# Performance work log

Measured on AMD Instinct MI355X. Metric: run time of the kernel, lower is better.

Reference implementation:

```python
import jax, jax.numpy as jnp
import numpy as np

B_, L_, D_, N_ = 4, 4096, 64, 16
DT = 0.1
EPS = 1e-6


def _complex_log(x):
    # log|x| (clamped) + i*pi for negative entries, matching torch impl
    real = jnp.log(jnp.maximum(jnp.abs(x), EPS))
    imag = jnp.where(x < 0, jnp.float32(np.pi), jnp.float32(0.0))
    return jax.lax.complex(real, imag)


def _clogaddexp(a, b):
    # stable complex log(exp(a)+exp(b)) using max of real parts
    m = jnp.maximum(a.real, b.real)
    return jnp.log(jnp.exp(a - m) + jnp.exp(b - m)) + m


def _clogcumsumexp(x, axis):
    return jax.lax.associative_scan(_clogaddexp, x, axis=axis)


def setup_inputs() -> dict:
    key = jax.random.key(0)
    ks = jax.random.split(key, 6)
    x = jax.random.normal(ks[0], (B_, L_, D_), jnp.float32)
    s = 1.0 / np.sqrt(D_)
    Wb = jax.random.uniform(ks[1], (N_, D_), jnp.float32, -s, s)
    bb = jax.random.uniform(ks[2], (N_,), jnp.float32, -s, s)
    Wc = jax.random.uniform(ks[3], (N_, D_), jnp.float32, -s, s)
    bc = jax.random.uniform(ks[4], (N_,), jnp.float32, -s, s)
    Wd = jax.random.uniform(ks[5], (1, D_), jnp.float32, -s, s)
    bd = jnp.zeros((1,), jnp.float32)
    # S4D-Real init: A_n = -(n+1), repeated over input_dim rows -> (D, N)
    A = jnp.tile(-(jnp.arange(N_, dtype=jnp.float32) + 1.0)[None, :], (D_, 1))
    return {"x": x, "A": A, "Wb": Wb, "bb": bb, "Wc": Wc, "bc": bc,
            "Wd": Wd, "bd": bd}


def reference(x, A, Wb, bb, Wc, bc, Wd, bd):
    # projections: (b,l,n)
    Bm = x @ Wb.T + bb
    Cm = x @ Wc.T + bc
    # delta network: softplus(linear(x)) + dt, broadcast to input_dim
    delta = jax.nn.softplus(x @ Wd.T + bd) + DT            # (b,l,1)
    dt = jnp.broadcast_to(delta, x.shape)                  # (b,l,d)
    # discretize
    tmp = A * dt[..., None]                                # (b,l,d,n)
    A_bar = jnp.exp(tmp)
    delta_B = jnp.einsum('bld,bln->bldn', dt, Bm)
    B_bar = (A_bar - 1.0) * delta_B / (tmp + EPS)
    term2 = B_bar * x[..., None]                           # (b,l,d,n)
    # parallel scan via complex log-cumsum-exp trick
    log_a = _complex_log(A_bar)
    log_b = _complex_log(term2)
    a_star = jnp.cumsum(log_a, axis=1)                     # (b,l,d,n) complex
    t = _clogcumsumexp(log_b - a_star, axis=1)
    scan = jnp.exp(a_star + t).real                        # (b,l,d,n)
    return jnp.sum(scan * Cm[:, :, None, :], axis=-1)      # (b,l,d)
```

## Files before the change

### kernel.cpp

```cpp
#include <hip/hip_runtime.h>

#define B_ 4
#define L_ 4096
#define D_ 64
#define N_ 16
#define CHUNK 32
#define NCHUNK (L_ / CHUNK)

constexpr float DT_  = 0.1f;
constexpr float EPS_ = 1e-6f;

__global__ __launch_bounds__(64) void proj_kernel(
    const float* __restrict__ x,  const float* __restrict__ A,
    const float* __restrict__ Wb, const float* __restrict__ bb,
    const float* __restrict__ Wc, const float* __restrict__ bc,
    const float* __restrict__ Wd, const float* __restrict__ bd,
    float* __restrict__ P, float* __restrict__ Cm)
{
    const int bl   = blockIdx.x;
    const int lane = threadIdx.x;

    float xd = x[(size_t)bl * D_ + lane];
    __shared__ float xs[D_];
    xs[lane] = xd;

    float p = xd * Wd[lane];
    #pragma unroll
    for (int m = 32; m >= 1; m >>= 1) p += __shfl_xor(p, m, 64);
    float z = p + bd[0];
    float delta = fmaxf(z, 0.0f) + log1pf(expf(-fabsf(z))) + DT_;

    __syncthreads();

    if (lane < 32) {
        const int n = lane & 15;
        const float* W  = (lane < 16) ? Wb : Wc;
        float acc = (lane < 16) ? bb[n] : bc[n];
        #pragma unroll
        for (int d = 0; d < D_; d++) acc += xs[d] * W[n * D_ + d];

        if (lane < 16) {
            float An  = A[n];
            float tmp = An * delta;
            float a   = expf(tmp);
            float g   = (a - 1.0f) * delta * acc / (tmp + EPS_);
            P[(size_t)bl * 32 + n]      = a;
            P[(size_t)bl * 32 + 16 + n] = g;
        } else {
            Cm[(size_t)bl * 16 + n] = acc;
        }
    }
}

__global__ __launch_bounds__(64) void scan_local(
    const float* __restrict__ x, const float* __restrict__ P,
    float* __restrict__ S, float* __restrict__ Cdec)
{
    const int b = blockIdx.x / NCHUNK;
    const int c = blockIdx.x % NCHUNK;
    const int d = threadIdx.x;

    float h[N_], cum[N_];
    #pragma unroll
    for (int n = 0; n < N_; n++) { h[n] = 0.0f; cum[n] = 1.0f; }

    const int l0 = c * CHUNK;
    for (int l = l0; l < l0 + CHUNK; l++) {
        const int base = b * L_ + l;
        float xd = x[(size_t)base * D_ + d];
        const float* pp = P + (size_t)base * 32;
        #pragma unroll
        for (int n = 0; n < N_; n++) {
            float a = pp[n];
            float g = pp[16 + n];
            h[n]   = a * h[n] + g * xd;
            cum[n] *= a;
        }
    }

    const int sbase = (b * NCHUNK + c) * N_;
    #pragma unroll
    for (int n = 0; n < N_; n++)
        S[(size_t)(sbase + n) * D_ + d] = h[n];
    if (d == 0) {
        #pragma unroll
        for (int n = 0; n < N_; n++) Cdec[sbase + n] = cum[n];
    }
}

__global__ __launch_bounds__(256) void combine(
    float* __restrict__ S, const float* __restrict__ Cdec)
{
    const int g = blockIdx.x * 256 + threadIdx.x;
    const int b = g / (N_ * D_);
    const int r = g % (N_ * D_);
    const int n = r / D_;
    const int d = r % D_;

    float run = 0.0f;
    for (int c = 0; c < NCHUNK; c++) {
        const size_t idx = (size_t)((b * NCHUNK + c) * N_ + n) * D_ + d;
        float s = S[idx];
        S[idx] = run;
        run = Cdec[(b * NCHUNK + c) * N_ + n] * run + s;
    }
}

__global__ __launch_bounds__(64) void scan_out(
    const float* __restrict__ x, const float* __restrict__ P,
    const float* __restrict__ Cmat, const float* __restrict__ S,
    float* __restrict__ out)
{
    const int b = blockIdx.x / NCHUNK;
    const int c = blockIdx.x % NCHUNK;
    const int d = threadIdx.x;

    float h[N_];
    const int sbase = (b * NCHUNK + c) * N_;
    #pragma unroll
    for (int n = 0; n < N_; n++)
        h[n] = S[(size_t)(sbase + n) * D_ + d];

    const int l0 = c * CHUNK;
    for (int l = l0; l < l0 + CHUNK; l++) {
        const int base = b * L_ + l;
        float xd = x[(size_t)base * D_ + d];
        const float* pp = P + (size_t)base * 32;
        const float* cc = Cmat + (size_t)base * 16;
        float acc = 0.0f;
        #pragma unroll
        for (int n = 0; n < N_; n++) {
            float a = pp[n];
            float g = pp[16 + n];
            h[n] = a * h[n] + g * xd;
            acc += cc[n] * h[n];
        }
        out[(size_t)base * D_ + d] = acc;
    }
}

extern "C" void kernel_launch(void* const* d_in, const int* in_sizes, int n_in,
                              void* d_out, int out_size, void* d_ws, size_t ws_size,
                              hipStream_t stream)
{
    const float* x  = (const float*)d_in[0];
    const float* A  = (const float*)d_in[1];
    const float* Wb = (const float*)d_in[2];
    const float* bb = (const float*)d_in[3];
    const float* Wc = (const float*)d_in[4];
    const float* bc = (const float*)d_in[5];
    const float* Wd = (const float*)d_in[6];
    const float* bd = (const float*)d_in[7];
    float* out = (float*)d_out;

    float* P    = (float*)d_ws;
    float* Cm   = P  + (size_t)B_ * L_ * 32;
    float* S    = Cm + (size_t)B_ * L_ * 16;
    float* Cdec = S  + (size_t)B_ * NCHUNK * N_ * D_;

    proj_kernel<<<B_ * L_, 64, 0, stream>>>(x, A, Wb, bb, Wc, bc, Wd, bd, P, Cm);
    scan_local<<<B_ * NCHUNK, 64, 0, stream>>>(x, P, S, Cdec);
    combine<<<(B_ * N_ * D_) / 256, 256, 0, stream>>>(S, Cdec);
    scan_out<<<B_ * NCHUNK, 64, 0, stream>>>(x, P, Cm, S, out);
}
```

Before: 123.8 us.

## Stage chunk inputs in LDS, register-cache weights, and batch positions in projection

```diff
diff --git a/kernel.cpp b/kernel.cpp
--- a/kernel.cpp
+++ b/kernel.cpp
@@ -6,6 +6,9 @@
 #define N_ 16
 #define CHUNK 32
 #define NCHUNK (L_ / CHUNK)
+#define TOTCHUNK (B_ * NCHUNK)
+#define POS (B_ * L_)
+#define POS_PER_BLK 8
 
 constexpr float DT_  = 0.1f;
 constexpr float EPS_ = 1e-6f;
@@ -17,37 +20,58 @@
     const float* __restrict__ Wd, const float* __restrict__ bd,
     float* __restrict__ P, float* __restrict__ Cm)
 {
-    const int bl   = blockIdx.x;
     const int lane = threadIdx.x;
-
-    float xd = x[(size_t)bl * D_ + lane];
+    const int o    = lane & 31;
+    const int h2   = lane >> 5;
     __shared__ float xs[D_];
-    xs[lane] = xd;
-
-    float p = xd * Wd[lane];
-    #pragma unroll
-    for (int m = 32; m >= 1; m >>= 1) p += __shfl_xor(p, m, 64);
-    float z = p + bd[0];
-    float delta = fmaxf(z, 0.0f) + log1pf(expf(-fabsf(z))) + DT_;
-
-    __syncthreads();
-
-    if (lane < 32) {
-        const int n = lane & 15;
-        const float* W  = (lane < 16) ? Wb : Wc;
-        float acc = (lane < 16) ? bb[n] : bc[n];
-        #pragma unroll
-        for (int d = 0; d < D_; d++) acc += xs[d] * W[n * D_ + d];
+
+    float wreg[32];
+    const float* Wrow = (o < 16) ? (Wb + o * D_) : (Wc + (o - 16) * D_);
+    const float4* w4p = (const float4*)(Wrow + h2 * 32);
+    #pragma unroll
+    for (int j = 0; j < 8; j++) {
+        float4 w4 = w4p[j];
+        wreg[4*j+0] = w4.x; wreg[4*j+1] = w4.y;
+        wreg[4*j+2] = w4.z; wreg[4*j+3] = w4.w;
+    }
+    const float wd   = Wd[lane];
+    const float bd0  = bd[0];
+    const float An   = A[lane & 15];
+    const float bias = (o < 16) ? bb[o] : bc[o - 16];
+
+    const int p0 = blockIdx.x * POS_PER_BLK;
+    for (int p = p0; p < p0 + POS_PER_BLK; p++) {
+        float xd = x[(size_t)p * D_ + lane];
+
+        float r = xd * wd;
+        #pragma unroll
+        for (int m = 32; m >= 1; m >>= 1) r += __shfl_xor(r, m, 64);
+        float z = r + bd0;
+        float delta = fmaxf(z, 0.0f) + log1pf(expf(-fabsf(z))) + DT_;
+
+        __syncthreads();
+        xs[lane] = xd;
+        __syncthreads();
+
+        float acc = 0.0f;
+        const float4* xs4 = (const float4*)(xs + h2 * 32);
+        #pragma unroll
+        for (int j = 0; j < 8; j++) {
+            float4 v = xs4[j];
+            acc += v.x * wreg[4*j+0] + v.y * wreg[4*j+1]
+                 + v.z * wreg[4*j+2] + v.w * wreg[4*j+3];
+        }
+        acc += __shfl_xor(acc, 32, 64);
 
         if (lane < 16) {
-            float An  = A[n];
+            float Bm  = acc + bias;
             float tmp = An * delta;
             float a   = expf(tmp);
-            float g   = (a - 1.0f) * delta * acc / (tmp + EPS_);
-            P[(size_t)bl * 32 + n]      = a;
-            P[(size_t)bl * 32 + 16 + n] = g;
-        } else {
-            Cm[(size_t)bl * 16 + n] = acc;
+            float g   = (a - 1.0f) * delta * Bm / (tmp + EPS_);
+            P[(size_t)p * 32 + lane]      = a;
+            P[(size_t)p * 32 + 16 + lane] = g;
+        } else if (lane < 32) {
+            Cm[(size_t)p * 16 + (lane - 16)] = acc + bias;
         }
     }
 }
@@ -56,53 +80,68 @@
     const float* __restrict__ x, const float* __restrict__ P,
     float* __restrict__ S, float* __restrict__ Cdec)
 {
-    const int b = blockIdx.x / NCHUNK;
-    const int c = blockIdx.x % NCHUNK;
+    const int gc    = blockIdx.x;
+    const int batch = gc / NCHUNK;
+    const int c     = gc % NCHUNK;
+    const int lane  = threadIdx.x;
+    const int base0 = batch * L_ + c * CHUNK;
+
+    __shared__ float xs[CHUNK * D_];
+    __shared__ float ag[CHUNK * 32];
+
+    const float4* xg  = (const float4*)(x + (size_t)base0 * D_);
+    float4*       xsv = (float4*)xs;
+    #pragma unroll
+    for (int i = 0; i < 8; i++) xsv[i * 64 + lane] = xg[i * 64 + lane];
+    const float4* pg  = (const float4*)(P + (size_t)base0 * 32);
+    float4*       agv = (float4*)ag;
+    #pragma unroll
+    for (int i = 0; i < 4; i++) agv[i * 64 + lane] = pg[i * 64 + lane];
+    __syncthreads();
+
+    float h[N_], cum[N_];
+    #pragma unroll
+    for (int n = 0; n < N_; n++) { h[n] = 0.0f; cum[n] = 1.0f; }
+
+    for (int s = 0; s < CHUNK; s++) {
+        float xd = xs[s * D_ + lane];
+        const float4* row = (const float4*)(ag + s * 32);
+        #pragma unroll
+        for (int q = 0; q < 4; q++) {
+            float4 a4 = row[q];
+            float4 g4 = row[4 + q];
+            h[4*q+0] = a4.x * h[4*q+0] + g4.x * xd;  cum[4*q+0] *= a4.x;
+            h[4*q+1] = a4.y * h[4*q+1] + g4.y * xd;  cum[4*q+1] *= a4.y;
+            h[4*q+2] = a4.z * h[4*q+2] + g4.z * xd;  cum[4*q+2] *= a4.z;
+            h[4*q+3] = a4.w * h[4*q+3] + g4.w * xd;  cum[4*q+3] *= a4.w;
+        }
+    }
+
+    #pragma unroll
+    for (int n = 0; n < N_; n++)
+        S[(size_t)(gc * N_ + n) * D_ + lane] = h[n];
+    if (lane == 0) {
+        #pragma unroll
+        for (int n = 0; n < N_; n++) Cdec[gc * N_ + n] = cum[n];
+    }
+}
+
+__global__ __launch_bounds__(64) void combine(
+    float* __restrict__ S, const float* __restrict__ Cdec)
+{
+    const int b = blockIdx.x >> 4;
+    const int n = blockIdx.x & 15;
     const int d = threadIdx.x;
 
-    float h[N_], cum[N_];
-    #pragma unroll
-    for (int n = 0; n < N_; n++) { h[n] = 0.0f; cum[n] = 1.0f; }
-
-    const int l0 = c * CHUNK;
-    for (int l = l0; l < l0 + CHUNK; l++) {
-        const int base = b * L_ + l;
-        float xd = x[(size_t)base * D_ + d];
-        const float* pp = P + (size_t)base * 32;
-        #pragma unroll
-        for (int n = 0; n < N_; n++) {
-            float a = pp[n];
-            float g = pp[16 + n];
-            h[n]   = a * h[n] + g * xd;
-            cum[n] *= a;
-        }
-    }
-
-    const int sbase = (b * NCHUNK + c) * N_;
-    #pragma unroll
-    for (int n = 0; n < N_; n++)
-        S[(size_t)(sbase + n) * D_ + d] = h[n];
-    if (d == 0) {
-        #pragma unroll
-        for (int n = 0; n < N_; n++) Cdec[sbase + n] = cum[n];
-    }
-}
-
-__global__ __launch_bounds__(256) void combine(
-    float* __restrict__ S, const float* __restrict__ Cdec)
-{
-    const int g = blockIdx.x * 256 + threadIdx.x;
-    const int b = g / (N_ * D_);
-    const int r = g % (N_ * D_);
-    const int n = r / D_;
-    const int d = r % D_;
-
     float run = 0.0f;
+    #pragma unroll 4
     for (int c = 0; c < NCHUNK; c++) {
-        const size_t idx = (size_t)((b * NCHUNK + c) * N_ + n) * D_ + d;
+        const int    gc  = b * NCHUNK + c;
+        const size_t idx = (size_t)(gc * N_ + n) * D_ + d;
         float s = S[idx];
+        float a = Cdec[gc * N_ + n];
         S[idx] = run;
-        run = Cdec[(b * NCHUNK + c) * N_ + n] * run + s;
+        run = a * run + s;
     }
 }
 
@@ -111,31 +150,51 @@
     const float* __restrict__ Cmat, const float* __restrict__ S,
     float* __restrict__ out)
 {
-    const int b = blockIdx.x / NCHUNK;
-    const int c = blockIdx.x % NCHUNK;
-    const int d = threadIdx.x;
+    const int gc    = blockIdx.x;
+    const int batch = gc / NCHUNK;
+    const int c     = gc % NCHUNK;
+    const int lane  = threadIdx.x;
+    const int base0 = batch * L_ + c * CHUNK;
+
+    __shared__ float xs[CHUNK * D_];
+    __shared__ float ag[CHUNK * 32];
+    __shared__ float cm[CHUNK * N_];
+
+    const float4* xg  = (const float4*)(x + (size_t)base0 * D_);
+    float4*       xsv = (float4*)xs;
+    #pragma unroll
+    for (int i = 0; i < 8; i++) xsv[i * 64 + lane] = xg[i * 64 + lane];
+    const float4* pg  = (const float4*)(P + (size_t)base0 * 32);
+    float4*       agv = (float4*)ag;
+    #pragma unroll
+    for (int i = 0; i < 4; i++) agv[i * 64 + lane] = pg[i * 64 + lane];
+    const float4* cg  = (const float4*)(Cmat + (size_t)base0 * 16);
+    float4*       cmv = (float4*)cm;
+    #pragma unroll
+    for (int i = 0; i < 2; i++) cmv[i * 64 + lane] = cg[i * 64 + lane];
+    __syncthreads();
 
     float h[N_];
-    const int sbase = (b * NCHUNK + c) * N_;
     #pragma unroll
     for (int n = 0; n < N_; n++)
-        h[n] = S[(size_t)(sbase + n) * D_ + d];
-
-    const int l0 = c * CHUNK;
-    for (int l = l0; l < l0 + CHUNK; l++) {
-        const int base = b * L_ + l;
-        float xd = x[(size_t)base * D_ + d];
-        const float* pp = P + (size_t)base * 32;
-        const float* cc = Cmat + (size_t)base * 16;
+        h[n] = S[(size_t)(gc * N_ + n) * D_ + lane];
+
+    for (int s = 0; s < CHUNK; s++) {
+        float xd = xs[s * D_ + lane];
+        const float4* row = (const float4*)(ag + s * 32);
+        const float4* crw = (const float4*)(cm + s * 16);
         float acc = 0.0f;
         #pragma unroll
-        for (int n = 0; n < N_; n++) {
-            float a = pp[n];
-            float g = pp[16 + n];
-            h[n] = a * h[n] + g * xd;
-            acc += cc[n] * h[n];
-        }
-        out[(size_t)base * D_ + d] = acc;
+        for (int q = 0; q < 4; q++) {
+            float4 a4 = row[q];
+            float4 g4 = row[4 + q];
+            float4 c4 = crw[q];
+            h[4*q+0] = a4.x * h[4*q+0] + g4.x * xd;  acc += c4.x * h[4*q+0];
+            h[4*q+1] = a4.y * h[4*q+1] + g4.y * xd;  acc += c4.y * h[4*q+1];
+            h[4*q+2] = a4.z * h[4*q+2] + g4.z * xd;  acc += c4.z * h[4*q+2];
+            h[4*q+3] = a4.w * h[4*q+3] + g4.w * xd;  acc += c4.w * h[4*q+3];
+        }
+        out[(size_t)(base0 + s) * D_ + lane] = acc;
     }
 }
 
@@ -156,10 +215,10 @@
     float* P    = (float*)d_ws;
     float* Cm   = P  + (size_t)B_ * L_ * 32;
     float* S    = Cm + (size_t)B_ * L_ * 16;
-    float* Cdec = S  + (size_t)B_ * NCHUNK * N_ * D_;
-
-    proj_kernel<<<B_ * L_, 64, 0, stream>>>(x, A, Wb, bb, Wc, bc, Wd, bd, P, Cm);
-    scan_local<<<B_ * NCHUNK, 64, 0, stream>>>(x, P, S, Cdec);
-    combine<<<(B_ * N_ * D_) / 256, 256, 0, stream>>>(S, Cdec);
-    scan_out<<<B_ * NCHUNK, 64, 0, stream>>>(x, P, Cm, S, out);
-}
+    float* Cdec = S  + (size_t)TOTCHUNK * N_ * D_;
+
+    proj_kernel<<<POS / POS_PER_BLK, 64, 0, stream>>>(x, A, Wb, bb, Wc, bc, Wd, bd, P, Cm);
+    scan_local<<<TOTCHUNK, 64, 0, stream>>>(x, P, S, Cdec);
+    combine<<<B_ * N_, 64, 0, stream>>>(S, Cdec);
+    scan_out<<<TOTCHUNK, 64, 0, stream>>>(x, P, Cm, S, out);
+}
```

After: 115.9 us. 6.3% less time.
